# Kernel tuning notes

Hardware: AMD Instinct MI355X
Metric: run time of the kernel (lower is better)

The kernel has to match this reference:

```python
import jax, jax.numpy as jnp
import numpy as np

N = 35          # nodes (hardcoded by x.repeat(35,1,1))
V = 4           # edge views
D1, D2, D3 = 512, 256, 128


def _full_graph_edges():
    # fully connected, no self loops, COO [2, E], E = 35*34
    src, dst = np.meshgrid(np.arange(N), np.arange(N), indexing='ij')
    mask = src != dst
    return np.stack([src[mask], dst[mask]], axis=0).astype(np.int64)


def setup_inputs() -> dict:
    key = jax.random.key(0)
    ks = jax.random.split(key, 8)
    E = N * (N - 1)
    edge_index = jnp.asarray(_full_graph_edges())
    s1, s2, s3 = 1.0 / np.sqrt(V), 1.0 / np.sqrt(V), 1.0 / np.sqrt(V)
    return {
        'x': jnp.ones((N, 1), jnp.float32),
        'edge_attr': jax.random.uniform(ks[0], (E, V), jnp.float32),
        'edge_index': edge_index,
        'mlp1_w': jax.random.normal(ks[1], (V, 1 * D1), jnp.float32) * s1,
        'mlp1_b': jnp.zeros((1 * D1,), jnp.float32),
        'root1': jax.random.normal(ks[2], (1, D1), jnp.float32),
        'bias1': jnp.zeros((D1,), jnp.float32),
        'mlp2_w': jax.random.normal(ks[3], (V, D1 * D2), jnp.float32) * s2,
        'mlp2_b': jnp.zeros((D1 * D2,), jnp.float32),
        'root2': jax.random.normal(ks[4], (D1, D2), jnp.float32) / np.sqrt(D1),
        'bias2': jnp.zeros((D2,), jnp.float32),
        'mlp3_w': jax.random.normal(ks[5], (V, D2 * D3), jnp.float32) * s3,
        'mlp3_b': jnp.zeros((D2 * D3,), jnp.float32),
        'root3': jax.random.normal(ks[6], (D2, D3), jnp.float32) / np.sqrt(D2),
        'bias3': jnp.zeros((D3,), jnp.float32),
    }


def _nnconv(x, edge_attr, src, dst, mlp_w, mlp_b, root, bias, in_c, out_c):
    # edge MLP -> per-edge weight matrix [E, in_c, out_c]
    w = jax.nn.relu(edge_attr @ mlp_w + mlp_b).reshape(-1, in_c, out_c)
    # gather source feats, per-edge matmul: [E, out_c]
    msg = jnp.einsum('ei,eio->eo', x[src], w)
    # scatter-mean to targets
    agg = jax.ops.segment_sum(msg, dst, num_segments=N)
    cnt = jax.ops.segment_sum(jnp.ones_like(msg[:, 0]), dst, num_segments=N)
    agg = agg / jnp.maximum(cnt, 1.0)[:, None]
    return agg + x @ root + bias


def reference(x, edge_attr, edge_index, mlp1_w, mlp1_b, root1, bias1,
              mlp2_w, mlp2_b, root2, bias2, mlp3_w, mlp3_b, root3, bias3):
    src, dst = edge_index[0], edge_index[1]
    h = jax.nn.relu(_nnconv(x, edge_attr, src, dst, mlp1_w, mlp1_b, root1, bias1, 1, D1))
    h = jax.nn.relu(_nnconv(h, edge_attr, src, dst, mlp2_w, mlp2_b, root2, bias2, D1, D2))
    h = jax.nn.relu(_nnconv(h, edge_attr, src, dst, mlp3_w, mlp3_b, root3, bias3, D2, D3))
    # cbt[a, i] = sum_f |h[i, f] - h[a, f]|   (repeat / transpose / abs / sum)
    cbt = jnp.sum(jnp.abs(h[None, :, :] - h[:, None, :]), axis=2)
    return cbt
```

## Files before the change

### kernel.cpp

```cpp
#include <hip/hip_runtime.h>

#define NN 35

typedef float v2f __attribute__((ext_vector_type(2)));

__device__ __forceinline__ v2f pk_fma(v2f a, v2f b, v2f c) {
#if __has_builtin(__builtin_elementwise_fma)
    return __builtin_elementwise_fma(a, b, c);
#else
    v2f d; d.x = fmaf(a.x, b.x, c.x); d.y = fmaf(a.y, b.y, c.y); return d;
#endif
}
__device__ __forceinline__ v2f pk_relu(v2f a) {
    v2f d; d.x = fmaxf(a.x, 0.f); d.y = fmaxf(a.y, 0.f); return d;
}
__device__ __forceinline__ v2f pk_splat(float s) {
    v2f d; d.x = s; d.y = s; return d;
}
__device__ __forceinline__ v2f pk_make(float a, float b) {
    v2f d; d.x = a; d.y = b; return d;
}


__global__ __launch_bounds__(512)
void layer1_kernel(const float* __restrict__ x,
                   const float* __restrict__ ea,
                   const float* __restrict__ W1, const float* __restrict__ b1,
                   const float* __restrict__ root1, const float* __restrict__ bias1,
                   float* __restrict__ h1,
                   float* __restrict__ aggz)
{
    const int d = blockIdx.x;
    const int o = threadIdx.x;
    const int gtid = d * 512 + o;
    if (gtid < 35 * 384) aggz[gtid] = 0.f;

    const float w0 = W1[o], w1 = W1[512 + o], w2 = W1[1024 + o], w3 = W1[1536 + o];
    const float bb = b1[o];
    float sum = 0.f;
#pragma unroll
    for (int s = 0; s < NN; ++s) {
        if (s == d) continue;
        const float4 a = ((const float4*)ea)[s * 34 + (d < s ? d : d - 1)];
        float w = fmaf(a.x, w0, fmaf(a.y, w1, fmaf(a.z, w2, fmaf(a.w, w3, bb))));
        sum = fmaf(x[s], fmaxf(w, 0.f), sum);
    }
    h1[gtid] = fmaxf(sum * (1.f / 34.f) + x[d] * root1[o] + bias1[o], 0.f);
}

__global__ __launch_bounds__(256, 2)
void edge2_kernel(const float* __restrict__ h,
                  const float* __restrict__ ea,
                  const float* __restrict__ W,
                  const float* __restrict__ bias,
                  const float* __restrict__ root,
                  float* __restrict__ agg)
{
    const int d  = blockIdx.x;
    const int c  = blockIdx.y;
    const int i0 = c * 16;
    const int o  = threadIdx.x;

    __shared__ __align__(16) float hs[35][16];
    __shared__ float4 as[34];

    if (o < 35) {
        const int s = (o < 34) ? (o + (o >= d ? 1 : 0)) : d;
        const float4* hp = (const float4*)(h + (size_t)s * 512 + i0);
#pragma unroll
        for (int k = 0; k < 4; ++k) ((float4*)hs[o])[k] = hp[k];
    }
    if (o >= 64 && o < 98) {
        const int j = o - 64;
        const int s = j + (j >= d ? 1 : 0);
        as[j] = ((const float4*)ea)[s * 34 + (d < s ? d : d - 1)];
    }
    __syncthreads();

    v2f W0[8], W1[8], W2[8], W3[8], BB[8], RR[8];
#pragma unroll
    for (int p = 0; p < 8; ++p) {
        const size_t b0 = (size_t)(i0 + 2 * p) * 256 + o;
        const size_t b1 = b0 + 256;
        W0[p] = pk_make(W[b0],          W[b1]);
        W1[p] = pk_make(W[131072 + b0], W[131072 + b1]);
        W2[p] = pk_make(W[262144 + b0], W[262144 + b1]);
        W3[p] = pk_make(W[393216 + b0], W[393216 + b1]);
        BB[p] = pk_make(bias[b0],       bias[b1]);
        RR[p] = pk_make(root[b0],       root[b1]);
    }

    v2f acc0 = pk_splat(0.f), acc1 = pk_splat(0.f);
#pragma unroll 2
    for (int j = 0; j < 34; ++j) {
        const float4 a = as[j];
        const v2f ax = pk_splat(a.x), ay = pk_splat(a.y);
        const v2f az = pk_splat(a.z), aw = pk_splat(a.w);
#pragma unroll
        for (int k = 0; k < 4; ++k) {
            const float4 hv = ((const float4*)hs[j])[k];
            const v2f h01 = pk_make(hv.x, hv.y);
            const v2f h23 = pk_make(hv.z, hv.w);
            {
                const int p = k * 2;
                v2f w = pk_fma(ax, W0[p], pk_fma(ay, W1[p],
                        pk_fma(az, W2[p], pk_fma(aw, W3[p], BB[p]))));
                acc0 = pk_fma(h01, pk_relu(w), acc0);
            }
            {
                const int p = k * 2 + 1;
                v2f w = pk_fma(ax, W0[p], pk_fma(ay, W1[p],
                        pk_fma(az, W2[p], pk_fma(aw, W3[p], BB[p]))));
                acc1 = pk_fma(h23, pk_relu(w), acc1);
            }
        }
    }
    v2f racc = pk_splat(0.f);
#pragma unroll
    for (int k = 0; k < 4; ++k) {
        const float4 hv = ((const float4*)hs[34])[k];
        racc = pk_fma(pk_make(hv.x, hv.y), RR[k * 2],     racc);
        racc = pk_fma(pk_make(hv.z, hv.w), RR[k * 2 + 1], racc);
    }
    const float acc = acc0.x + acc0.y + acc1.x + acc1.y;
    atomicAdd(&agg[d * 256 + o], acc * (1.f / 34.f) + (racc.x + racc.y));
}

__global__ __launch_bounds__(128, 2)
void edge3_kernel(const float* __restrict__ agg2,
                  const float* __restrict__ bias2,
                  const float* __restrict__ ea,
                  const float* __restrict__ W,
                  const float* __restrict__ bias,
                  const float* __restrict__ root,
                  float* __restrict__ agg)
{
    const int d  = blockIdx.x;
    const int c  = blockIdx.y;
    const int i0 = c * 8;
    const int o  = threadIdx.x;

    __shared__ __align__(16) float hs[35][8];
    __shared__ float4 as[34];

    if (o < 70) {
        const int r = o >> 1, k = o & 1;
        const int s = (r < 34) ? (r + (r >= d ? 1 : 0)) : d;
        float4 v = ((const float4*)(agg2 + (size_t)s * 256 + i0))[k];
        const float4 bv = ((const float4*)(bias2 + i0))[k];
        v.x = fmaxf(v.x + bv.x, 0.f);
        v.y = fmaxf(v.y + bv.y, 0.f);
        v.z = fmaxf(v.z + bv.z, 0.f);
        v.w = fmaxf(v.w + bv.w, 0.f);
        ((float4*)hs[r])[k] = v;
    }
    if (o >= 94) {
        const int j = o - 94;
        const int s = j + (j >= d ? 1 : 0);
        as[j] = ((const float4*)ea)[s * 34 + (d < s ? d : d - 1)];
    }
    __syncthreads();

    v2f W0[4], W1[4], W2[4], W3[4], BB[4], RR[4];
#pragma unroll
    for (int p = 0; p < 4; ++p) {
        const size_t b0 = (size_t)(i0 + 2 * p) * 128 + o;
        const size_t b1 = b0 + 128;
        W0[p] = pk_make(W[b0],         W[b1]);
        W1[p] = pk_make(W[32768 + b0], W[32768 + b1]);
        W2[p] = pk_make(W[65536 + b0], W[65536 + b1]);
        W3[p] = pk_make(W[98304 + b0], W[98304 + b1]);
        BB[p] = pk_make(bias[b0],      bias[b1]);
        RR[p] = pk_make(root[b0],      root[b1]);
    }

    v2f acc0 = pk_splat(0.f), acc1 = pk_splat(0.f);
#pragma unroll 2
    for (int j = 0; j < 34; ++j) {
        const float4 a = as[j];
        const v2f ax = pk_splat(a.x), ay = pk_splat(a.y);
        const v2f az = pk_splat(a.z), aw = pk_splat(a.w);
#pragma unroll
        for (int k = 0; k < 2; ++k) {
            const float4 hv = ((const float4*)hs[j])[k];
            const v2f h01 = pk_make(hv.x, hv.y);
            const v2f h23 = pk_make(hv.z, hv.w);
            {
                const int p = k * 2;
                v2f w = pk_fma(ax, W0[p], pk_fma(ay, W1[p],
                        pk_fma(az, W2[p], pk_fma(aw, W3[p], BB[p]))));
                acc0 = pk_fma(h01, pk_relu(w), acc0);
            }
            {
                const int p = k * 2 + 1;
                v2f w = pk_fma(ax, W0[p], pk_fma(ay, W1[p],
                        pk_fma(az, W2[p], pk_fma(aw, W3[p], BB[p]))));
                acc1 = pk_fma(h23, pk_relu(w), acc1);
            }
        }
    }
    v2f racc = pk_splat(0.f);
#pragma unroll
    for (int k = 0; k < 2; ++k) {
        const float4 hv = ((const float4*)hs[34])[k];
        racc = pk_fma(pk_make(hv.x, hv.y), RR[k * 2],     racc);
        racc = pk_fma(pk_make(hv.z, hv.w), RR[k * 2 + 1], racc);
    }
    const float acc = acc0.x + acc0.y + acc1.x + acc1.y;
    atomicAdd(&agg[d * 128 + o], acc * (1.f / 34.f) + (racc.x + racc.y));
}

__global__ __launch_bounds__(256)
void cbt_kernel(const float* __restrict__ agg3,
                const float* __restrict__ bias3,
                float* __restrict__ out)
{
    const int wv = blockIdx.x * 4 + (threadIdx.x >> 6);
    const int lane = threadIdx.x & 63;
    if (wv >= NN * NN) return;
    const int a_ = wv / NN, i_ = wv % NN;
    float s = 0.f;
#pragma unroll
    for (int q = 0; q < 2; ++q) {
        const int f = lane + q * 64;
        const float bb = bias3[f];
        const float hi = fmaxf(agg3[i_ * 128 + f] + bb, 0.f);
        const float ha = fmaxf(agg3[a_ * 128 + f] + bb, 0.f);
        s += fabsf(hi - ha);
    }
#pragma unroll
    for (int off = 32; off > 0; off >>= 1)
        s += __shfl_xor(s, off, 64);
    if (lane == 0) out[wv] = s;
}

extern "C" void kernel_launch(void* const* d_in, const int* in_sizes, int n_in,
                              void* d_out, int out_size, void* d_ws, size_t ws_size,
                              hipStream_t stream) {
    const float* x      = (const float*)d_in[0];
    const float* ea     = (const float*)d_in[1];
    const float* mlp1_w = (const float*)d_in[3];
    const float* mlp1_b = (const float*)d_in[4];
    const float* root1  = (const float*)d_in[5];
    const float* bias1  = (const float*)d_in[6];
    const float* mlp2_w = (const float*)d_in[7];
    const float* mlp2_b = (const float*)d_in[8];
    const float* root2  = (const float*)d_in[9];
    const float* bias2  = (const float*)d_in[10];
    const float* mlp3_w = (const float*)d_in[11];
    const float* mlp3_b = (const float*)d_in[12];
    const float* root3  = (const float*)d_in[13];
    const float* bias3  = (const float*)d_in[14];
    float* out = (float*)d_out;

    float* ws   = (float*)d_ws;
    float* agg2 = ws;
    float* agg3 = agg2 + 35 * 256;
    float* h1   = agg3 + 35 * 128;

    layer1_kernel<<<NN, 512, 0, stream>>>(x, ea, mlp1_w, mlp1_b, root1, bias1, h1, agg2);
    edge2_kernel<<<dim3(NN, 32), 256, 0, stream>>>(h1, ea, mlp2_w, mlp2_b, root2, agg2);
    edge3_kernel<<<dim3(NN, 32), 128, 0, stream>>>(agg2, bias2, ea, mlp3_w, mlp3_b, root3, agg3);
    cbt_kernel<<<(NN * NN + 3) / 4, 256, 0, stream>>>(agg3, bias3, out);
}
```

Measured before the change: 131.2 us.

## Fuse all layers into one persistent kernel with software grid barriers

Replaces the four per-stage launches with a small init kernel plus one persistent kernel of 512 blocks. Stages are separated by an atomic-counter grid barrier, and intermediates pass through agent-scope atomic loads and stores. The work split is also retiled: layer 2 now uses 8-row chunks across 2240 tiles, and layer 3 uses two thread groups of 128 per block. This removes kernel launch gaps and tail effects, at the cost of barrier spin time and a risk of deadlock if the 512 blocks are not all co-resident.

New measurement: 289.9 us. 2.21x slower.

```diff
diff --git a/kernel.cpp b/kernel.cpp
--- a/kernel.cpp
+++ b/kernel.cpp
@@ -1,6 +1,7 @@
 #include <hip/hip_runtime.h>
 
 #define NN 35
+#define GRID 512
 
 typedef float v2f __attribute__((ext_vector_type(2)));
 
@@ -14,224 +15,235 @@
 __device__ __forceinline__ v2f pk_relu(v2f a) {
     v2f d; d.x = fmaxf(a.x, 0.f); d.y = fmaxf(a.y, 0.f); return d;
 }
-__device__ __forceinline__ v2f pk_splat(float s) {
-    v2f d; d.x = s; d.y = s; return d;
-}
-__device__ __forceinline__ v2f pk_make(float a, float b) {
-    v2f d; d.x = a; d.y = b; return d;
-}
-
-
-__global__ __launch_bounds__(512)
-void layer1_kernel(const float* __restrict__ x,
-                   const float* __restrict__ ea,
-                   const float* __restrict__ W1, const float* __restrict__ b1,
-                   const float* __restrict__ root1, const float* __restrict__ bias1,
-                   float* __restrict__ h1,
-                   float* __restrict__ aggz)
+__device__ __forceinline__ v2f pk_splat(float s) { v2f d; d.x = s; d.y = s; return d; }
+__device__ __forceinline__ v2f pk_make(float a, float b) { v2f d; d.x = a; d.y = b; return d; }
+
+__device__ __forceinline__ float agld(const float* p) {
+    return __hip_atomic_load(p, __ATOMIC_RELAXED, __HIP_MEMORY_SCOPE_AGENT);
+}
+__device__ __forceinline__ void agst(float* p, float v) {
+    __hip_atomic_store(p, v, __ATOMIC_RELAXED, __HIP_MEMORY_SCOPE_AGENT);
+}
+
+
+__global__ __launch_bounds__(256)
+void init_kernel(float* __restrict__ ws) {
+    const int i = blockIdx.x * 256 + threadIdx.x;
+    if (i < 35 * 384) ws[i] = 0.f;
+    if (i < 2) ((unsigned*)(ws + 31360))[i] = 0u;
+}
+
+__device__ __forceinline__ void gbar(unsigned* cnt, unsigned* gen, unsigned nb) {
+    __syncthreads();
+    if (threadIdx.x == 0) {
+        __threadfence();
+        const unsigned g = __hip_atomic_load(gen, __ATOMIC_RELAXED, __HIP_MEMORY_SCOPE_AGENT);
+        const unsigned a = __hip_atomic_fetch_add(cnt, 1u, __ATOMIC_ACQ_REL, __HIP_MEMORY_SCOPE_AGENT);
+        if (a == nb - 1u) {
+            __hip_atomic_store(cnt, 0u, __ATOMIC_RELAXED, __HIP_MEMORY_SCOPE_AGENT);
+            __hip_atomic_fetch_add(gen, 1u, __ATOMIC_RELEASE, __HIP_MEMORY_SCOPE_AGENT);
+        } else {
+            while (__hip_atomic_load(gen, __ATOMIC_RELAXED, __HIP_MEMORY_SCOPE_AGENT) == g)
+                __builtin_amdgcn_s_sleep(2);
+        }
+        __threadfence();
+    }
+    __syncthreads();
+}
+
+__global__ __launch_bounds__(256, 2)
+void fused_kernel(const float* __restrict__ x,
+                  const float* __restrict__ ea,
+                  const float* __restrict__ W1, const float* __restrict__ b1,
+                  const float* __restrict__ root1, const float* __restrict__ bias1,
+                  const float* __restrict__ W2, const float* __restrict__ b2,
+                  const float* __restrict__ root2, const float* __restrict__ bias2,
+                  const float* __restrict__ W3, const float* __restrict__ b3,
+                  const float* __restrict__ root3, const float* __restrict__ bias3,
+                  float* __restrict__ out,
+                  float* __restrict__ ws)
 {
-    const int d = blockIdx.x;
-    const int o = threadIdx.x;
-    const int gtid = d * 512 + o;
-    if (gtid < 35 * 384) aggz[gtid] = 0.f;
-
-    const float w0 = W1[o], w1 = W1[512 + o], w2 = W1[1024 + o], w3 = W1[1536 + o];
-    const float bb = b1[o];
-    float sum = 0.f;
-#pragma unroll
-    for (int s = 0; s < NN; ++s) {
-        if (s == d) continue;
-        const float4 a = ((const float4*)ea)[s * 34 + (d < s ? d : d - 1)];
-        float w = fmaf(a.x, w0, fmaf(a.y, w1, fmaf(a.z, w2, fmaf(a.w, w3, bb))));
-        sum = fmaf(x[s], fmaxf(w, 0.f), sum);
-    }
-    h1[gtid] = fmaxf(sum * (1.f / 34.f) + x[d] * root1[o] + bias1[o], 0.f);
-}
-
-__global__ __launch_bounds__(256, 2)
-void edge2_kernel(const float* __restrict__ h,
-                  const float* __restrict__ ea,
-                  const float* __restrict__ W,
-                  const float* __restrict__ bias,
-                  const float* __restrict__ root,
-                  float* __restrict__ agg)
-{
-    const int d  = blockIdx.x;
-    const int c  = blockIdx.y;
-    const int i0 = c * 16;
-    const int o  = threadIdx.x;
-
-    __shared__ __align__(16) float hs[35][16];
-    __shared__ float4 as[34];
-
-    if (o < 35) {
-        const int s = (o < 34) ? (o + (o >= d ? 1 : 0)) : d;
-        const float4* hp = (const float4*)(h + (size_t)s * 512 + i0);
-#pragma unroll
-        for (int k = 0; k < 4; ++k) ((float4*)hs[o])[k] = hp[k];
-    }
-    if (o >= 64 && o < 98) {
-        const int j = o - 64;
-        const int s = j + (j >= d ? 1 : 0);
-        as[j] = ((const float4*)ea)[s * 34 + (d < s ? d : d - 1)];
-    }
-    __syncthreads();
-
-    v2f W0[8], W1[8], W2[8], W3[8], BB[8], RR[8];
-#pragma unroll
-    for (int p = 0; p < 8; ++p) {
-        const size_t b0 = (size_t)(i0 + 2 * p) * 256 + o;
-        const size_t b1 = b0 + 256;
-        W0[p] = pk_make(W[b0],          W[b1]);
-        W1[p] = pk_make(W[131072 + b0], W[131072 + b1]);
-        W2[p] = pk_make(W[262144 + b0], W[262144 + b1]);
-        W3[p] = pk_make(W[393216 + b0], W[393216 + b1]);
-        BB[p] = pk_make(bias[b0],       bias[b1]);
-        RR[p] = pk_make(root[b0],       root[b1]);
-    }
-
-    v2f acc0 = pk_splat(0.f), acc1 = pk_splat(0.f);
-#pragma unroll 2
-    for (int j = 0; j < 34; ++j) {
-        const float4 a = as[j];
-        const v2f ax = pk_splat(a.x), ay = pk_splat(a.y);
-        const v2f az = pk_splat(a.z), aw = pk_splat(a.w);
-#pragma unroll
-        for (int k = 0; k < 4; ++k) {
-            const float4 hv = ((const float4*)hs[j])[k];
-            const v2f h01 = pk_make(hv.x, hv.y);
-            const v2f h23 = pk_make(hv.z, hv.w);
-            {
-                const int p = k * 2;
-                v2f w = pk_fma(ax, W0[p], pk_fma(ay, W1[p],
-                        pk_fma(az, W2[p], pk_fma(aw, W3[p], BB[p]))));
-                acc0 = pk_fma(h01, pk_relu(w), acc0);
-            }
-            {
-                const int p = k * 2 + 1;
-                v2f w = pk_fma(ax, W0[p], pk_fma(ay, W1[p],
-                        pk_fma(az, W2[p], pk_fma(aw, W3[p], BB[p]))));
-                acc1 = pk_fma(h23, pk_relu(w), acc1);
-            }
-        }
-    }
-    v2f racc = pk_splat(0.f);
-#pragma unroll
-    for (int k = 0; k < 4; ++k) {
-        const float4 hv = ((const float4*)hs[34])[k];
-        racc = pk_fma(pk_make(hv.x, hv.y), RR[k * 2],     racc);
-        racc = pk_fma(pk_make(hv.z, hv.w), RR[k * 2 + 1], racc);
-    }
-    const float acc = acc0.x + acc0.y + acc1.x + acc1.y;
-    atomicAdd(&agg[d * 256 + o], acc * (1.f / 34.f) + (racc.x + racc.y));
-}
-
-__global__ __launch_bounds__(128, 2)
-void edge3_kernel(const float* __restrict__ agg2,
-                  const float* __restrict__ bias2,
-                  const float* __restrict__ ea,
-                  const float* __restrict__ W,
-                  const float* __restrict__ bias,
-                  const float* __restrict__ root,
-                  float* __restrict__ agg)
-{
-    const int d  = blockIdx.x;
-    const int c  = blockIdx.y;
-    const int i0 = c * 8;
-    const int o  = threadIdx.x;
+    float* agg2 = ws;
+    float* agg3 = ws + 8960;
+    float* h1   = ws + 13440;
+    unsigned* bar = (unsigned*)(ws + 31360);
+    const unsigned nb = gridDim.x;
+    const int thr = threadIdx.x;
 
     __shared__ __align__(16) float hs[35][8];
     __shared__ float4 as[34];
 
-    if (o < 70) {
-        const int r = o >> 1, k = o & 1;
-        const int s = (r < 34) ? (r + (r >= d ? 1 : 0)) : d;
-        float4 v = ((const float4*)(agg2 + (size_t)s * 256 + i0))[k];
-        const float4 bv = ((const float4*)(bias2 + i0))[k];
-        v.x = fmaxf(v.x + bv.x, 0.f);
-        v.y = fmaxf(v.y + bv.y, 0.f);
-        v.z = fmaxf(v.z + bv.z, 0.f);
-        v.w = fmaxf(v.w + bv.w, 0.f);
-        ((float4*)hs[r])[k] = v;
-    }
-    if (o >= 94) {
-        const int j = o - 94;
-        const int s = j + (j >= d ? 1 : 0);
-        as[j] = ((const float4*)ea)[s * 34 + (d < s ? d : d - 1)];
-    }
-    __syncthreads();
-
-    v2f W0[4], W1[4], W2[4], W3[4], BB[4], RR[4];
-#pragma unroll
-    for (int p = 0; p < 4; ++p) {
-        const size_t b0 = (size_t)(i0 + 2 * p) * 128 + o;
-        const size_t b1 = b0 + 128;
-        W0[p] = pk_make(W[b0],         W[b1]);
-        W1[p] = pk_make(W[32768 + b0], W[32768 + b1]);
-        W2[p] = pk_make(W[65536 + b0], W[65536 + b1]);
-        W3[p] = pk_make(W[98304 + b0], W[98304 + b1]);
-        BB[p] = pk_make(bias[b0],      bias[b1]);
-        RR[p] = pk_make(root[b0],      root[b1]);
-    }
-
-    v2f acc0 = pk_splat(0.f), acc1 = pk_splat(0.f);
+    for (int gt = blockIdx.x * 256 + thr; gt < 35 * 512; gt += gridDim.x * 256) {
+        const int d = gt >> 9, o = gt & 511;
+        const float w0 = W1[o], w1 = W1[512 + o], w2 = W1[1024 + o], w3 = W1[1536 + o];
+        const float bb = b1[o];
+        float sum = 0.f;
+#pragma unroll
+        for (int s = 0; s < NN; ++s) {
+            if (s == d) continue;
+            const float4 a = ((const float4*)ea)[s * 34 + (d < s ? d : d - 1)];
+            float w = fmaf(a.x, w0, fmaf(a.y, w1, fmaf(a.z, w2, fmaf(a.w, w3, bb))));
+            sum = fmaf(x[s], fmaxf(w, 0.f), sum);
+        }
+        agst(&h1[gt], fmaxf(sum * (1.f / 34.f) + x[d] * root1[o] + bias1[o], 0.f));
+    }
+
+    gbar(bar, bar + 1, nb);
+
+    for (int t = blockIdx.x; t < 35 * 64; t += gridDim.x) {
+        const int d  = t % 35;
+        const int c  = t / 35;
+        const int i0 = c * 8;
+        const int o  = thr;
+
+        __syncthreads();
+        if (thr < 70) {
+            const int r = thr >> 1, k = thr & 1;
+            const int s = (r < 34) ? (r + (r >= d ? 1 : 0)) : d;
+#pragma unroll
+            for (int q = 0; q < 4; ++q)
+                hs[r][k * 4 + q] = agld(&h1[s * 512 + i0 + k * 4 + q]);
+        }
+        if (thr >= 70 && thr < 104) {
+            const int j = thr - 70;
+            const int s = j + (j >= d ? 1 : 0);
+            as[j] = ((const float4*)ea)[s * 34 + (d < s ? d : d - 1)];
+        }
+        __syncthreads();
+
+        v2f Wv0[4], Wv1[4], Wv2[4], Wv3[4], BB[4], RR[4];
+#pragma unroll
+        for (int p = 0; p < 4; ++p) {
+            const size_t b0 = (size_t)(i0 + 2 * p) * 256 + o;
+            const size_t bq = b0 + 256;
+            Wv0[p] = pk_make(W2[b0],          W2[bq]);
+            Wv1[p] = pk_make(W2[131072 + b0], W2[131072 + bq]);
+            Wv2[p] = pk_make(W2[262144 + b0], W2[262144 + bq]);
+            Wv3[p] = pk_make(W2[393216 + b0], W2[393216 + bq]);
+            BB[p]  = pk_make(b2[b0],          b2[bq]);
+            RR[p]  = pk_make(root2[b0],       root2[bq]);
+        }
+
+        v2f acc0 = pk_splat(0.f), acc1 = pk_splat(0.f);
 #pragma unroll 2
-    for (int j = 0; j < 34; ++j) {
-        const float4 a = as[j];
-        const v2f ax = pk_splat(a.x), ay = pk_splat(a.y);
-        const v2f az = pk_splat(a.z), aw = pk_splat(a.w);
+        for (int j = 0; j < 34; ++j) {
+            const float4 a = as[j];
+            const v2f ax = pk_splat(a.x), ay = pk_splat(a.y);
+            const v2f az = pk_splat(a.z), aw = pk_splat(a.w);
+#pragma unroll
+            for (int k = 0; k < 2; ++k) {
+                const float4 hv = ((const float4*)hs[j])[k];
+                {
+                    const int p = k * 2;
+                    v2f w = pk_fma(ax, Wv0[p], pk_fma(ay, Wv1[p],
+                            pk_fma(az, Wv2[p], pk_fma(aw, Wv3[p], BB[p]))));
+                    acc0 = pk_fma(pk_make(hv.x, hv.y), pk_relu(w), acc0);
+                }
+                {
+                    const int p = k * 2 + 1;
+                    v2f w = pk_fma(ax, Wv0[p], pk_fma(ay, Wv1[p],
+                            pk_fma(az, Wv2[p], pk_fma(aw, Wv3[p], BB[p]))));
+                    acc1 = pk_fma(pk_make(hv.z, hv.w), pk_relu(w), acc1);
+                }
+            }
+        }
+        v2f racc = pk_splat(0.f);
 #pragma unroll
         for (int k = 0; k < 2; ++k) {
-            const float4 hv = ((const float4*)hs[j])[k];
-            const v2f h01 = pk_make(hv.x, hv.y);
-            const v2f h23 = pk_make(hv.z, hv.w);
+            const float4 hv = ((const float4*)hs[34])[k];
+            racc = pk_fma(pk_make(hv.x, hv.y), RR[k * 2],     racc);
+            racc = pk_fma(pk_make(hv.z, hv.w), RR[k * 2 + 1], racc);
+        }
+        const float acc = acc0.x + acc0.y + acc1.x + acc1.y;
+        atomicAdd(&agg2[d * 256 + o], acc * (1.f / 34.f) + (racc.x + racc.y));
+    }
+
+    gbar(bar, bar + 1, nb);
+
+    for (int t = blockIdx.x; t < 35 * 32; t += gridDim.x) {
+        const int d  = t % 35;
+        const int c  = t / 35;
+        const int i0 = c * 8;
+        const int o  = thr & 127;
+        const int g  = thr >> 7;
+
+        __syncthreads();
+        if (thr < 70) {
+            const int r = thr >> 1, k = thr & 1;
+            const int s = (r < 34) ? (r + (r >= d ? 1 : 0)) : d;
+#pragma unroll
+            for (int q = 0; q < 4; ++q) {
+                const int f = i0 + k * 4 + q;
+                hs[r][k * 4 + q] = fmaxf(agld(&agg2[s * 256 + f]) + bias2[f], 0.f);
+            }
+        }
+        if (thr >= 70 && thr < 104) {
+            const int j = thr - 70;
+            const int s = j + (j >= d ? 1 : 0);
+            as[j] = ((const float4*)ea)[s * 34 + (d < s ? d : d - 1)];
+        }
+        __syncthreads();
+
+        v2f Wv0[2], Wv1[2], Wv2[2], Wv3[2], BB[2], RR[2];
+#pragma unroll
+        for (int p = 0; p < 2; ++p) {
+            const size_t b0 = (size_t)(i0 + g * 4 + 2 * p) * 128 + o;
+            const size_t bq = b0 + 128;
+            Wv0[p] = pk_make(W3[b0],         W3[bq]);
+            Wv1[p] = pk_make(W3[32768 + b0], W3[32768 + bq]);
+            Wv2[p] = pk_make(W3[65536 + b0], W3[65536 + bq]);
+            Wv3[p] = pk_make(W3[98304 + b0], W3[98304 + bq]);
+            BB[p]  = pk_make(b3[b0],         b3[bq]);
+            RR[p]  = pk_make(root3[b0],      root3[bq]);
+        }
+
+        v2f acc0 = pk_splat(0.f), acc1 = pk_splat(0.f);
+#pragma unroll 2
+        for (int j = 0; j < 34; ++j) {
+            const float4 a = as[j];
+            const v2f ax = pk_splat(a.x), ay = pk_splat(a.y);
+            const v2f az = pk_splat(a.z), aw = pk_splat(a.w);
+            const float4 hv = ((const float4*)hs[j])[g];
             {
-                const int p = k * 2;
-                v2f w = pk_fma(ax, W0[p], pk_fma(ay, W1[p],
-                        pk_fma(az, W2[p], pk_fma(aw, W3[p], BB[p]))));
-                acc0 = pk_fma(h01, pk_relu(w), acc0);
+                v2f w = pk_fma(ax, Wv0[0], pk_fma(ay, Wv1[0],
+                        pk_fma(az, Wv2[0], pk_fma(aw, Wv3[0], BB[0]))));
+                acc0 = pk_fma(pk_make(hv.x, hv.y), pk_relu(w), acc0);
             }
             {
-                const int p = k * 2 + 1;
-                v2f w = pk_fma(ax, W0[p], pk_fma(ay, W1[p],
-                        pk_fma(az, W2[p], pk_fma(aw, W3[p], BB[p]))));
-                acc1 = pk_fma(h23, pk_relu(w), acc1);
-            }
-        }
-    }
-    v2f racc = pk_splat(0.f);
-#pragma unroll
-    for (int k = 0; k < 2; ++k) {
-        const float4 hv = ((const float4*)hs[34])[k];
-        racc = pk_fma(pk_make(hv.x, hv.y), RR[k * 2],     racc);
-        racc = pk_fma(pk_make(hv.z, hv.w), RR[k * 2 + 1], racc);
-    }
-    const float acc = acc0.x + acc0.y + acc1.x + acc1.y;
-    atomicAdd(&agg[d * 128 + o], acc * (1.f / 34.f) + (racc.x + racc.y));
-}
-
-__global__ __launch_bounds__(256)
-void cbt_kernel(const float* __restrict__ agg3,
-                const float* __restrict__ bias3,
-                float* __restrict__ out)
-{
-    const int wv = blockIdx.x * 4 + (threadIdx.x >> 6);
-    const int lane = threadIdx.x & 63;
-    if (wv >= NN * NN) return;
-    const int a_ = wv / NN, i_ = wv % NN;
-    float s = 0.f;
-#pragma unroll
-    for (int q = 0; q < 2; ++q) {
-        const int f = lane + q * 64;
-        const float bb = bias3[f];
-        const float hi = fmaxf(agg3[i_ * 128 + f] + bb, 0.f);
-        const float ha = fmaxf(agg3[a_ * 128 + f] + bb, 0.f);
-        s += fabsf(hi - ha);
-    }
-#pragma unroll
-    for (int off = 32; off > 0; off >>= 1)
-        s += __shfl_xor(s, off, 64);
-    if (lane == 0) out[wv] = s;
+                v2f w = pk_fma(ax, Wv0[1], pk_fma(ay, Wv1[1],
+                        pk_fma(az, Wv2[1], pk_fma(aw, Wv3[1], BB[1]))));
+                acc1 = pk_fma(pk_make(hv.z, hv.w), pk_relu(w), acc1);
+            }
+        }
+        v2f racc = pk_splat(0.f);
+        {
+            const float4 hv = ((const float4*)hs[34])[g];
+            racc = pk_fma(pk_make(hv.x, hv.y), RR[0], racc);
+            racc = pk_fma(pk_make(hv.z, hv.w), RR[1], racc);
+        }
+        const float acc = acc0.x + acc0.y + acc1.x + acc1.y;
+        atomicAdd(&agg3[d * 128 + o], acc * (1.f / 34.f) + (racc.x + racc.y));
+    }
+
+    gbar(bar, bar + 1, nb);
+
+    const int lane = thr & 63;
+    for (int wv = blockIdx.x * 4 + (thr >> 6); wv < NN * NN; wv += gridDim.x * 4) {
+        const int a_ = wv / NN, i_ = wv % NN;
+        float s = 0.f;
+#pragma unroll
+        for (int q = 0; q < 2; ++q) {
+            const int f = lane + q * 64;
+            const float bb = bias3[f];
+            const float hi = fmaxf(agld(&agg3[i_ * 128 + f]) + bb, 0.f);
+            const float ha = fmaxf(agld(&agg3[a_ * 128 + f]) + bb, 0.f);
+            s += fabsf(hi - ha);
+        }
+#pragma unroll
+        for (int off = 32; off > 0; off >>= 1)
+            s += __shfl_xor(s, off, 64);
+        if (lane == 0) out[wv] = s;
+    }
 }
 
 extern "C" void kernel_launch(void* const* d_in, const int* in_sizes, int n_in,
@@ -252,14 +264,12 @@
     const float* root3  = (const float*)d_in[13];
     const float* bias3  = (const float*)d_in[14];
     float* out = (float*)d_out;
-
-    float* ws   = (float*)d_ws;
-    float* agg2 = ws;
-    float* agg3 = agg2 + 35 * 256;
-    float* h1   = agg3 + 35 * 128;
-
-    layer1_kernel<<<NN, 512, 0, stream>>>(x, ea, mlp1_w, mlp1_b, root1, bias1, h1, agg2);
-    edge2_kernel<<<dim3(NN, 32), 256, 0, stream>>>(h1, ea, mlp2_w, mlp2_b, root2, agg2);
-    edge3_kernel<<<dim3(NN, 32), 128, 0, stream>>>(agg2, bias2, ea, mlp3_w, mlp3_b, root3, agg3);
-    cbt_kernel<<<(NN * NN + 3) / 4, 256, 0, stream>>>(agg3, bias3, out);
-}
+    float* ws  = (float*)d_ws;
+
+    init_kernel<<<53, 256, 0, stream>>>(ws);
+    fused_kernel<<<GRID, 256, 0, stream>>>(x, ea,
+                                           mlp1_w, mlp1_b, root1, bias1,
+                                           mlp2_w, mlp2_b, root2, bias2,
+                                           mlp3_w, mlp3_b, root3, bias3,
+                                           out, ws);
+}
```

## Fuse cbt distance computation into edge3 via last-block atomic counter

Applied to the files above, without the earlier changes.

Removes the separate cbt kernel launch by having the last-finishing edge3 block, found through a global atomic counter zeroed in layer1, compute the pairwise L1 distance matrix. It exploits symmetry to compute only the upper triangle and writes both entries. The edge2 inner loop is also restructured to load two float4 of h per step. The trade-off is that the final reduction runs serially on a single 128-thread block with atomic loads, in exchange for saving one launch and its gap.

Measured after the change: 191.9 us. 46.2% more time.

```diff
diff --git a/kernel.cpp b/kernel.cpp
--- a/kernel.cpp
+++ b/kernel.cpp
@@ -14,11 +14,11 @@
 __device__ __forceinline__ v2f pk_relu(v2f a) {
     v2f d; d.x = fmaxf(a.x, 0.f); d.y = fmaxf(a.y, 0.f); return d;
 }
-__device__ __forceinline__ v2f pk_splat(float s) {
-    v2f d; d.x = s; d.y = s; return d;
-}
-__device__ __forceinline__ v2f pk_make(float a, float b) {
-    v2f d; d.x = a; d.y = b; return d;
+__device__ __forceinline__ v2f pk_splat(float s) { v2f d; d.x = s; d.y = s; return d; }
+__device__ __forceinline__ v2f pk_make(float a, float b) { v2f d; d.x = a; d.y = b; return d; }
+
+__device__ __forceinline__ float agld(const float* p) {
+    return __hip_atomic_load(p, __ATOMIC_RELAXED, __HIP_MEMORY_SCOPE_AGENT);
 }
 
 
@@ -34,6 +34,7 @@
     const int o = threadIdx.x;
     const int gtid = d * 512 + o;
     if (gtid < 35 * 384) aggz[gtid] = 0.f;
+    if (gtid == 35 * 384) ((unsigned*)aggz)[13440] = 0u;
 
     const float w0 = W1[o], w1 = W1[512 + o], w2 = W1[1024 + o], w3 = W1[1536 + o];
     const float bb = b1[o];
@@ -77,17 +78,17 @@
     }
     __syncthreads();
 
-    v2f W0[8], W1[8], W2[8], W3[8], BB[8], RR[8];
+    v2f Wv0[8], Wv1[8], Wv2[8], Wv3[8], BB[8], RR[8];
 #pragma unroll
     for (int p = 0; p < 8; ++p) {
         const size_t b0 = (size_t)(i0 + 2 * p) * 256 + o;
-        const size_t b1 = b0 + 256;
-        W0[p] = pk_make(W[b0],          W[b1]);
-        W1[p] = pk_make(W[131072 + b0], W[131072 + b1]);
-        W2[p] = pk_make(W[262144 + b0], W[262144 + b1]);
-        W3[p] = pk_make(W[393216 + b0], W[393216 + b1]);
-        BB[p] = pk_make(bias[b0],       bias[b1]);
-        RR[p] = pk_make(root[b0],       root[b1]);
+        const size_t bq = b0 + 256;
+        Wv0[p] = pk_make(W[b0],          W[bq]);
+        Wv1[p] = pk_make(W[131072 + b0], W[131072 + bq]);
+        Wv2[p] = pk_make(W[262144 + b0], W[262144 + bq]);
+        Wv3[p] = pk_make(W[393216 + b0], W[393216 + bq]);
+        BB[p]  = pk_make(bias[b0],       bias[bq]);
+        RR[p]  = pk_make(root[b0],       root[bq]);
     }
 
     v2f acc0 = pk_splat(0.f), acc1 = pk_splat(0.f);
@@ -97,21 +98,32 @@
         const v2f ax = pk_splat(a.x), ay = pk_splat(a.y);
         const v2f az = pk_splat(a.z), aw = pk_splat(a.w);
 #pragma unroll
-        for (int k = 0; k < 4; ++k) {
-            const float4 hv = ((const float4*)hs[j])[k];
-            const v2f h01 = pk_make(hv.x, hv.y);
-            const v2f h23 = pk_make(hv.z, hv.w);
-            {
-                const int p = k * 2;
-                v2f w = pk_fma(ax, W0[p], pk_fma(ay, W1[p],
-                        pk_fma(az, W2[p], pk_fma(aw, W3[p], BB[p]))));
-                acc0 = pk_fma(h01, pk_relu(w), acc0);
-            }
-            {
-                const int p = k * 2 + 1;
-                v2f w = pk_fma(ax, W0[p], pk_fma(ay, W1[p],
-                        pk_fma(az, W2[p], pk_fma(aw, W3[p], BB[p]))));
-                acc1 = pk_fma(h23, pk_relu(w), acc1);
+        for (int k = 0; k < 2; ++k) {
+            const float4 hv = ((const float4*)hs[j])[k * 2];
+            const float4 hv2 = ((const float4*)hs[j])[k * 2 + 1];
+            {
+                const int p = k * 4;
+                v2f w = pk_fma(ax, Wv0[p], pk_fma(ay, Wv1[p],
+                        pk_fma(az, Wv2[p], pk_fma(aw, Wv3[p], BB[p]))));
+                acc0 = pk_fma(pk_make(hv.x, hv.y), pk_relu(w), acc0);
+            }
+            {
+                const int p = k * 4 + 1;
+                v2f w = pk_fma(ax, Wv0[p], pk_fma(ay, Wv1[p],
+                        pk_fma(az, Wv2[p], pk_fma(aw, Wv3[p], BB[p]))));
+                acc1 = pk_fma(pk_make(hv.z, hv.w), pk_relu(w), acc1);
+            }
+            {
+                const int p = k * 4 + 2;
+                v2f w = pk_fma(ax, Wv0[p], pk_fma(ay, Wv1[p],
+                        pk_fma(az, Wv2[p], pk_fma(aw, Wv3[p], BB[p]))));
+                acc0 = pk_fma(pk_make(hv2.x, hv2.y), pk_relu(w), acc0);
+            }
+            {
+                const int p = k * 4 + 3;
+                v2f w = pk_fma(ax, Wv0[p], pk_fma(ay, Wv1[p],
+                        pk_fma(az, Wv2[p], pk_fma(aw, Wv3[p], BB[p]))));
+                acc1 = pk_fma(pk_make(hv2.z, hv2.w), pk_relu(w), acc1);
             }
         }
     }
@@ -127,13 +139,16 @@
 }
 
 __global__ __launch_bounds__(128, 2)
-void edge3_kernel(const float* __restrict__ agg2,
-                  const float* __restrict__ bias2,
-                  const float* __restrict__ ea,
-                  const float* __restrict__ W,
-                  const float* __restrict__ bias,
-                  const float* __restrict__ root,
-                  float* __restrict__ agg)
+void edge3cbt_kernel(const float* __restrict__ agg2,
+                     const float* __restrict__ bias2,
+                     const float* __restrict__ ea,
+                     const float* __restrict__ W,
+                     const float* __restrict__ bias,
+                     const float* __restrict__ root,
+                     const float* __restrict__ bias3,
+                     float* __restrict__ agg,
+                     unsigned* __restrict__ cnt,
+                     float* __restrict__ out)
 {
     const int d  = blockIdx.x;
     const int c  = blockIdx.y;
@@ -142,6 +157,7 @@
 
     __shared__ __align__(16) float hs[35][8];
     __shared__ float4 as[34];
+    __shared__ unsigned lastflag;
 
     if (o < 70) {
         const int r = o >> 1, k = o & 1;
@@ -161,17 +177,17 @@
     }
     __syncthreads();
 
-    v2f W0[4], W1[4], W2[4], W3[4], BB[4], RR[4];
+    v2f Wv0[4], Wv1[4], Wv2[4], Wv3[4], BB[4], RR[4];
 #pragma unroll
     for (int p = 0; p < 4; ++p) {
         const size_t b0 = (size_t)(i0 + 2 * p) * 128 + o;
-        const size_t b1 = b0 + 128;
-        W0[p] = pk_make(W[b0],         W[b1]);
-        W1[p] = pk_make(W[32768 + b0], W[32768 + b1]);
-        W2[p] = pk_make(W[65536 + b0], W[65536 + b1]);
-        W3[p] = pk_make(W[98304 + b0], W[98304 + b1]);
-        BB[p] = pk_make(bias[b0],      bias[b1]);
-        RR[p] = pk_make(root[b0],      root[b1]);
+        const size_t bq = b0 + 128;
+        Wv0[p] = pk_make(W[b0],         W[bq]);
+        Wv1[p] = pk_make(W[32768 + b0], W[32768 + bq]);
+        Wv2[p] = pk_make(W[65536 + b0], W[65536 + bq]);
+        Wv3[p] = pk_make(W[98304 + b0], W[98304 + bq]);
+        BB[p]  = pk_make(bias[b0],      bias[bq]);
+        RR[p]  = pk_make(root[b0],      root[bq]);
     }
 
     v2f acc0 = pk_splat(0.f), acc1 = pk_splat(0.f);
@@ -183,19 +199,17 @@
 #pragma unroll
         for (int k = 0; k < 2; ++k) {
             const float4 hv = ((const float4*)hs[j])[k];
-            const v2f h01 = pk_make(hv.x, hv.y);
-            const v2f h23 = pk_make(hv.z, hv.w);
             {
                 const int p = k * 2;
-                v2f w = pk_fma(ax, W0[p], pk_fma(ay, W1[p],
-                        pk_fma(az, W2[p], pk_fma(aw, W3[p], BB[p]))));
-                acc0 = pk_fma(h01, pk_relu(w), acc0);
+                v2f w = pk_fma(ax, Wv0[p], pk_fma(ay, Wv1[p],
+                        pk_fma(az, Wv2[p], pk_fma(aw, Wv3[p], BB[p]))));
+                acc0 = pk_fma(pk_make(hv.x, hv.y), pk_relu(w), acc0);
             }
             {
                 const int p = k * 2 + 1;
-                v2f w = pk_fma(ax, W0[p], pk_fma(ay, W1[p],
-                        pk_fma(az, W2[p], pk_fma(aw, W3[p], BB[p]))));
-                acc1 = pk_fma(h23, pk_relu(w), acc1);
+                v2f w = pk_fma(ax, Wv0[p], pk_fma(ay, Wv1[p],
+                        pk_fma(az, Wv2[p], pk_fma(aw, Wv3[p], BB[p]))));
+                acc1 = pk_fma(pk_make(hv.z, hv.w), pk_relu(w), acc1);
             }
         }
     }
@@ -208,30 +222,32 @@
     }
     const float acc = acc0.x + acc0.y + acc1.x + acc1.y;
     atomicAdd(&agg[d * 128 + o], acc * (1.f / 34.f) + (racc.x + racc.y));
-}
-
-__global__ __launch_bounds__(256)
-void cbt_kernel(const float* __restrict__ agg3,
-                const float* __restrict__ bias3,
-                float* __restrict__ out)
-{
-    const int wv = blockIdx.x * 4 + (threadIdx.x >> 6);
-    const int lane = threadIdx.x & 63;
-    if (wv >= NN * NN) return;
-    const int a_ = wv / NN, i_ = wv % NN;
-    float s = 0.f;
-#pragma unroll
-    for (int q = 0; q < 2; ++q) {
-        const int f = lane + q * 64;
-        const float bb = bias3[f];
-        const float hi = fmaxf(agg3[i_ * 128 + f] + bb, 0.f);
-        const float ha = fmaxf(agg3[a_ * 128 + f] + bb, 0.f);
-        s += fabsf(hi - ha);
-    }
-#pragma unroll
-    for (int off = 32; off > 0; off >>= 1)
-        s += __shfl_xor(s, off, 64);
-    if (lane == 0) out[wv] = s;
+
+    __syncthreads();
+    if (o == 0) {
+        __threadfence();
+        lastflag = (atomicAdd(cnt, 1u) == 35u * 32u - 1u) ? 1u : 0u;
+    }
+    __syncthreads();
+    if (!lastflag) return;
+    __threadfence();
+
+    for (int idx = o; idx < NN * NN; idx += 128) {
+        const int a_ = idx / NN, i_ = idx % NN;
+        if (a_ > i_) continue;
+        const float* ra = agg + a_ * 128;
+        const float* ri = agg + i_ * 128;
+        float s = 0.f;
+#pragma unroll 16
+        for (int f = 0; f < 128; ++f) {
+            const float bb = bias3[f];
+            const float va = fmaxf(agld(&ra[f]) + bb, 0.f);
+            const float vi = fmaxf(agld(&ri[f]) + bb, 0.f);
+            s += fabsf(vi - va);
+        }
+        out[a_ * NN + i_] = s;
+        out[i_ * NN + a_] = s;
+    }
 }
 
 extern "C" void kernel_launch(void* const* d_in, const int* in_sizes, int n_in,
@@ -255,11 +271,12 @@
 
     float* ws   = (float*)d_ws;
     float* agg2 = ws;
-    float* agg3 = agg2 + 35 * 256;
-    float* h1   = agg3 + 35 * 128;
-
-    layer1_kernel<<<NN, 512, 0, stream>>>(x, ea, mlp1_w, mlp1_b, root1, bias1, h1, agg2);
+    float* agg3 = ws + 8960;
+    unsigned* cnt = (unsigned*)(ws + 13440);
+    float* h1   = ws + 13444;
+
+    layer1_kernel<<<NN, 512, 0, stream>>>(x, ea, mlp1_w, mlp1_b, root1, bias1, h1, ws);
     edge2_kernel<<<dim3(NN, 32), 256, 0, stream>>>(h1, ea, mlp2_w, mlp2_b, root2, agg2);
-    edge3_kernel<<<dim3(NN, 32), 128, 0, stream>>>(agg2, bias2, ea, mlp3_w, mlp3_b, root3, agg3);
-    cbt_kernel<<<(NN * NN + 3) / 4, 256, 0, stream>>>(agg3, bias3, out);
-}
+    edge3cbt_kernel<<<dim3(NN, 32), 128, 0, stream>>>(agg2, bias2, ea, mlp3_w, mlp3_b,
+                                                      root3, bias3, agg3, cnt, out);
+}
```
